# Performance work log

Hardware: AMD Instinct MI355X
Metric: run time of the kernel (lower is better)

## Reference

```python
import jax, jax.numpy as jnp
import numpy as np

B = 16384
D1 = 256
D2 = 256
D_FF = 1024
N_BINS = 16
TAIL = 3.0
MIN_VAL = 1e-3
MIN_TOTAL = N_BINS * MIN_VAL
TAIL_CONST = float(np.log(np.exp(1.0 - MIN_VAL) - 1.0))
D_OUT = (3 * N_BINS - 1) * D2  # 12032


def setup_inputs() -> dict:
    key = jax.random.key(0)
    ks = jax.random.split(key, 8)
    s = lambda fan: 1.0 / np.sqrt(fan)
    return {
        'x1': jax.random.normal(ks[0], (B, D1), jnp.float32),
        'x2': jax.random.normal(ks[1], (B, D2), jnp.float32),
        'W0': jax.random.normal(ks[2], (D1, D_FF), jnp.float32) * s(D1),
        'b0': jnp.zeros((D_FF,), jnp.float32),
        'W1': jax.random.normal(ks[3], (D_FF, D_FF), jnp.float32) * s(D_FF),
        'b1': jnp.zeros((D_FF,), jnp.float32),
        'W2': jax.random.normal(ks[4], (D_FF, D_OUT), jnp.float32) * s(D_FF),
        'b2': jnp.zeros((D_OUT,), jnp.float32),
    }


def _rqs_forward(x, wu, hu, du):
    # x: [B, D2]; wu, hu: [B, D2, N_BINS]; du: [B, D2, N_BINS-1]
    widths = MIN_VAL + (1.0 - MIN_TOTAL) * jax.nn.softmax(wu, axis=-1)
    heights = MIN_VAL + (1.0 - MIN_TOTAL) * jax.nn.softmax(hu, axis=-1)
    cw = jnp.cumsum(widths, axis=-1)
    cw = jnp.concatenate([jnp.zeros_like(cw[..., :1]), cw], axis=-1)
    cw = 2.0 * TAIL * cw - TAIL  # x bin edges in [-TAIL, TAIL], [B,D2,N_BINS+1]
    ch = jnp.cumsum(heights, axis=-1)
    ch = jnp.concatenate([jnp.zeros_like(ch[..., :1]), ch], axis=-1)
    ch = 2.0 * TAIL * ch - TAIL  # y bin edges
    w = cw[..., 1:] - cw[..., :-1]
    h = ch[..., 1:] - ch[..., :-1]
    # boundary derivatives padded so softplus(TAIL_CONST)+MIN_VAL == 1 (linear tails)
    pad = jnp.full_like(du[..., :1], TAIL_CONST)
    d = MIN_VAL + jax.nn.softplus(jnp.concatenate([pad, du, pad], axis=-1))  # [B,D2,N_BINS+1]
    inside = (x > -TAIL) & (x < TAIL)
    xc = jnp.clip(x, -TAIL, TAIL)
    # data-dependent bin search against interior edges
    idx = jnp.sum((xc[..., None] >= cw[..., 1:-1]).astype(jnp.int32), axis=-1)  # [B,D2]
    take = lambda a: jnp.take_along_axis(a, idx[..., None], axis=-1)[..., 0]
    xk = take(cw[..., :-1]); yk = take(ch[..., :-1])
    wk = take(w); hk = take(h)
    dk = take(d[..., :-1]); dk1 = take(d[..., 1:])
    sk = hk / wk
    theta = (xc - xk) / wk
    t1m = theta * (1.0 - theta)
    denom = sk + (dk + dk1 - 2.0 * sk) * t1m
    y = yk + hk * (sk * theta * theta + dk * t1m) / denom
    deriv = sk * sk * (dk1 * theta * theta + 2.0 * sk * t1m + dk * (1.0 - theta) ** 2) / (denom * denom)
    y = jnp.where(inside, y, x)            # identity tails
    logdet = jnp.where(inside, jnp.log(deriv), 0.0)
    return y, jnp.sum(logdet, axis=-1)     # [B,D2], [B]


def reference(x1, x2, W0, b0, W1, b1, W2, b2):
    # conditioner MLP: x1 -> spline parameters
    hdn = jax.nn.relu(x1 @ W0 + b0)
    hdn = jax.nn.relu(hdn @ W1 + b1)
    p = (hdn @ W2 + b2).reshape(-1, D2, 3 * N_BINS - 1)
    wu = p[..., :N_BINS]
    hu = p[..., N_BINS:2 * N_BINS]
    du = p[..., 2 * N_BINS:]
    y2, logdet = _rqs_forward(x2, wu, hu, du)
    return y2, logdet
```

## Files before the change

kernel.cpp:

```cpp
#include <hip/hip_runtime.h>
#include <math.h>

using u16 = unsigned short;
using bf16x8 = __attribute__((ext_vector_type(8))) short;
using f32x4  = __attribute__((ext_vector_type(4))) float;

#define DEV static __device__ __forceinline__

DEV u16 f2bf(float f) {
  union { float f; unsigned u; } v; v.f = f;
  unsigned u = v.u + 0x7fffu + ((v.u >> 16) & 1u);
  return (u16)(u >> 16);
}

DEV void gload16(const void* g, void* l) {
  __builtin_amdgcn_global_load_lds(
      (const __attribute__((address_space(1))) void*)g,
      (__attribute__((address_space(3))) void*)l, 16, 0, 0);
}

__global__ void k_conv_bf16(const float* __restrict__ in, u16* __restrict__ out, int n) {
  int i = blockIdx.x * 256 + threadIdx.x;
  if (i < n) out[i] = f2bf(in[i]);
}

__global__ void k_transconv(const float* __restrict__ in, u16* __restrict__ out,
                            int K, int Nin, int Nout, int pack) {
  __shared__ float t[32][33];
  int kb = blockIdx.x * 32, nb = blockIdx.y * 32;
  int tx = threadIdx.x & 31, ty = threadIdx.x >> 5;
  #pragma unroll
  for (int i = 0; i < 4; ++i) {
    int k = kb + ty + i * 8;
    int no = nb + tx;
    float v = 0.f;
    if (k < K && no < Nout) {
      if (pack) {
        int r = no % 48;
        if (r < 47) v = in[(size_t)k * Nin + (no / 48) * 47 + r];
      } else {
        v = in[(size_t)k * Nin + no];
      }
    }
    t[ty + i * 8][tx] = v;
  }
  __syncthreads();
  #pragma unroll
  for (int i = 0; i < 4; ++i) {
    int no = nb + ty + i * 8;
    int k = kb + tx;
    if (no < Nout && k < K) out[(size_t)no * K + k] = f2bf(t[tx][ty + i * 8]);
  }
}

__global__ __launch_bounds__(256)
void k_gemm_relu(const u16* __restrict__ A, const u16* __restrict__ Bt,
                 const float* __restrict__ bias, u16* __restrict__ C,
                 int N, int K) {
  constexpr int BM = 128, BN = 128, BK = 32;
  __shared__ __align__(16) u16 lds[(BM + BN) * BK];
  int tid = threadIdx.x, w = tid >> 6, lane = tid & 63;
  int bn = blockIdx.x, bm = blockIdx.y;
  int brow = bm * BM, bcol = bn * BN;
  int wm = w >> 1, wn = w & 1;
  int fr = lane & 15, fg = lane >> 4;
  f32x4 acc[4][4];
  #pragma unroll
  for (int i = 0; i < 4; ++i)
    #pragma unroll
    for (int j = 0; j < 4; ++j) acc[i][j] = (f32x4){0.f, 0.f, 0.f, 0.f};

  constexpr int ACH = BM * BK / 8;
  constexpr int CALLS = (BM + BN) * BK / 8 / 64;

  for (int kt = 0; kt < K; kt += BK) {
    for (int j = 0; j * 4 + w < CALLS; ++j) {
      int cb = (j * 4 + w) * 64;
      int c = cb + lane;
      const u16* g;
      if (c < ACH) {
        int row = c >> 2, c8 = c & 3;
        g = A + (size_t)(brow + row) * K + kt + c8 * 8;
      } else {
        int b = c - ACH;
        int nn = b >> 2, c8 = b & 3;
        g = Bt + (size_t)(bcol + nn) * K + kt + c8 * 8;
      }
      gload16(g, &lds[cb * 8]);
    }
    asm volatile("s_waitcnt vmcnt(0)" ::: "memory");
    __syncthreads();

    const u16* Al = lds;
    const u16* Bl = lds + BM * BK;
    bf16x8 af[4], bfr[4];
    #pragma unroll
    for (int mi = 0; mi < 4; ++mi)
      af[mi] = *(const bf16x8*)&Al[(wm * 64 + mi * 16 + fr) * BK + fg * 8];
    #pragma unroll
    for (int ni = 0; ni < 4; ++ni)
      bfr[ni] = *(const bf16x8*)&Bl[(wn * 64 + ni * 16 + fr) * BK + fg * 8];
    #pragma unroll
    for (int mi = 0; mi < 4; ++mi)
      #pragma unroll
      for (int ni = 0; ni < 4; ++ni)
        acc[mi][ni] = __builtin_amdgcn_mfma_f32_16x16x32_bf16(af[mi], bfr[ni], acc[mi][ni], 0, 0, 0);
    __syncthreads();
  }

  #pragma unroll
  for (int ni = 0; ni < 4; ++ni) {
    int col = bcol + wn * 64 + ni * 16 + fr;
    float bb = bias[col];
    #pragma unroll
    for (int mi = 0; mi < 4; ++mi) {
      #pragma unroll
      for (int q = 0; q < 4; ++q) {
        int row = brow + wm * 64 + mi * 16 + fg * 4 + q;
        float vv = acc[mi][ni][q] + bb;
        C[(size_t)row * N + col] = f2bf(vv > 0.f ? vv : 0.f);
      }
    }
  }
}

__global__ __launch_bounds__(256, 2)
void k_gemm3_fused(const u16* __restrict__ A, const u16* __restrict__ Bt,
                   const float* __restrict__ b2, const float* __restrict__ x2,
                   float* __restrict__ y2, float* __restrict__ ldpart) {
  extern __shared__ char smem[];
  const int tid = threadIdx.x, w = tid >> 6, lane = tid & 63;
  const int wm = w >> 1, wn = w & 1;
  const int fr = lane & 15, fg = lane >> 4;

  const int bid = blockIdx.x;
  const int bm = bid >> 6;
  const int bn = ((bid & 7) << 3) | ((bid >> 3) & 7);
  const int brow = bm * 128;

  const int csrc = (tid & 7) ^ ((tid >> 3) & 7);
  const u16* gA[4]; const u16* gB[6];
  #pragma unroll
  for (int k = 0; k < 4; ++k)
    gA[k] = A + (size_t)(brow + (tid >> 3) + 32 * k) * 1024 + csrc * 8;
  #pragma unroll
  for (int k = 0; k < 6; ++k)
    gB[k] = Bt + (size_t)(bn * 192 + (tid >> 3) + 32 * k) * 1024 + csrc * 8;

#define ISSUE_ALL(t1) {                                               \
    const size_t ko_ = (size_t)(t1) * 64;                             \
    char* pa_ = smem + ((t1) & 1) * 16384;                            \
    char* pb_ = smem + 32768 + ((t1) & 1) * 24576;                    \
    gload16(gA[0] + ko_, pa_ + tid * 16);                             \
    gload16(gA[1] + ko_, pa_ + tid * 16 + 4096);                      \
    gload16(gA[2] + ko_, pa_ + tid * 16 + 8192);                      \
    gload16(gA[3] + ko_, pa_ + tid * 16 + 12288);                     \
    gload16(gB[0] + ko_, pb_ + tid * 16);                             \
    gload16(gB[1] + ko_, pb_ + tid * 16 + 4096);                      \
    gload16(gB[2] + ko_, pb_ + tid * 16 + 8192);                      \
    gload16(gB[3] + ko_, pb_ + tid * 16 + 12288);                     \
    gload16(gB[4] + ko_, pb_ + tid * 16 + 16384);                     \
    gload16(gB[5] + ko_, pb_ + tid * 16 + 20480); }

  const int sc0 = ((fg ^ (fr & 7)) << 4);
  const int sc1 = (((4 + fg) ^ (fr & 7)) << 4);

  f32x4 acc[4][6];
  #pragma unroll
  for (int m = 0; m < 4; ++m)
    #pragma unroll
    for (int n = 0; n < 6; ++n) acc[m][n] = (f32x4){0.f, 0.f, 0.f, 0.f};

  ISSUE_ALL(0);
  asm volatile("s_waitcnt vmcnt(0)" ::: "memory");
  __syncthreads();

  for (int t = 0; t < 16; ++t) {
    if (t < 15) ISSUE_ALL(t + 1);
    const char* Ab = smem + (t & 1) * 16384;
    const char* Bb = smem + 32768 + (t & 1) * 24576;
    bf16x8 b0[6], b1[6];
    #pragma unroll
    for (int n = 0; n < 6; ++n) {
      const char* bp = Bb + (wn * 96 + n * 16 + fr) * 128;
      b0[n] = *(const bf16x8*)(bp + sc0);
      b1[n] = *(const bf16x8*)(bp + sc1);
    }
    __builtin_amdgcn_s_setprio(1);
    #pragma unroll
    for (int m = 0; m < 4; ++m) {
      const char* ap = Ab + (wm * 64 + m * 16 + fr) * 128;
      bf16x8 a0 = *(const bf16x8*)(ap + sc0);
      bf16x8 a1 = *(const bf16x8*)(ap + sc1);
      #pragma unroll
      for (int n = 0; n < 6; ++n) {
        acc[m][n] = __builtin_amdgcn_mfma_f32_16x16x32_bf16(a0, b0[n], acc[m][n], 0, 0, 0);
        acc[m][n] = __builtin_amdgcn_mfma_f32_16x16x32_bf16(a1, b1[n], acc[m][n], 0, 0, 0);
      }
    }
    __builtin_amdgcn_s_setprio(0);
    asm volatile("s_waitcnt vmcnt(0)" ::: "memory");
    __syncthreads();
  }

  float* ldacc = (float*)(smem + 50176);
  float* fl = (float*)smem;
  #pragma unroll
  for (int rh = 0; rh < 2; ++rh) {
    if (wm == rh) {
      #pragma unroll
      for (int m = 0; m < 4; ++m)
        #pragma unroll
        for (int n = 0; n < 6; ++n) {
          const int g = wn * 2 + (n >= 3 ? 1 : 0);
          const int ci = (n % 3) * 16 + fr;
          #pragma unroll
          for (int q = 0; q < 4; ++q)
            fl[g * 3136 + (m * 16 + fg * 4 + q) * 49 + ci] = acc[m][n][q];
        }
    }
    __syncthreads();
    {
      const int g = tid >> 6, r = tid & 63;
      const float* pr = fl + g * 3136 + r * 49;
      const int grow = brow + rh * 64 + r;
      const int d2 = bn * 4 + g;
      const float* bb = b2 + (size_t)d2 * 47;

      float wv[16], hv[16];
      #pragma unroll
      for (int j = 0; j < 16; ++j) wv[j] = pr[j] + bb[j];
      #pragma unroll
      for (int j = 0; j < 16; ++j) hv[j] = pr[16 + j] + bb[16 + j];

      float x = x2[(size_t)grow * 256 + d2];
      float xc = fminf(fmaxf(x, -3.f), 3.f);

      float mw = wv[0];
      #pragma unroll
      for (int j = 1; j < 16; ++j) mw = fmaxf(mw, wv[j]);
      float sw = 0.f;
      #pragma unroll
      for (int j = 0; j < 16; ++j) { wv[j] = __expf(wv[j] - mw); sw += wv[j]; }
      float scw = 0.984f / sw;

      float mh = hv[0];
      #pragma unroll
      for (int j = 1; j < 16; ++j) mh = fmaxf(mh, hv[j]);
      float sh = 0.f;
      #pragma unroll
      for (int j = 0; j < 16; ++j) { hv[j] = __expf(hv[j] - mh); sh += hv[j]; }
      float sch = 0.984f / sh;

      int idx = 0;
      float xk = -3.f, cum = 0.f;
      #pragma unroll
      for (int i = 1; i <= 15; ++i) {
        cum += 0.001f + wv[i - 1] * scw;
        float cwi = 6.f * cum - 3.f;
        if (xc >= cwi) { idx = i; xk = cwi; }
      }
      float yk = -3.f, cumh = 0.f;
      #pragma unroll
      for (int i = 1; i <= 15; ++i) {
        cumh += 0.001f + hv[i - 1] * sch;
        float chi = 6.f * cumh - 3.f;
        if (i == idx) yk = chi;
      }
      float wk = 1.f, hk = 1.f;
      #pragma unroll
      for (int i = 0; i < 16; ++i) {
        if (i == idx) {
          wk = 6.f * (0.001f + wv[i] * scw);
          hk = 6.f * (0.001f + hv[i] * sch);
        }
      }
      float dk = 1.f, dk1 = 1.f;
      #pragma unroll
      for (int i = 1; i <= 15; ++i) {
        float u = pr[32 + i - 1] + bb[32 + i - 1];
        float e = __expf(u);
        float dd = 0.001f + (u > 15.f ? u : log1pf(e));
        if (i == idx) dk = dd;
        if (i == idx + 1) dk1 = dd;
      }

      float sk = hk / wk;
      float th = (xc - xk) / wk;
      float om = 1.f - th;
      float t1m = th * om;
      float den = sk + (dk + dk1 - 2.f * sk) * t1m;
      float y = yk + hk * (sk * th * th + dk * t1m) / den;
      float deriv = sk * sk * (dk1 * th * th + 2.f * sk * t1m + dk * om * om) / (den * den);
      bool inside = (x > -3.f) && (x < 3.f);
      float yout = inside ? y : x;
      float ld = inside ? __logf(deriv) : 0.f;

      y2[(size_t)grow * 256 + d2] = yout;
      ldacc[(rh * 64 + r) * 4 + g] = ld;
    }
    __syncthreads();
  }

  if (tid < 128) {
    float s = ldacc[tid * 4] + ldacc[tid * 4 + 1] + ldacc[tid * 4 + 2] + ldacc[tid * 4 + 3];
    ldpart[(size_t)bn * 16384 + brow + tid] = s;
  }
}

__global__ void k_reduce_ld(const float* __restrict__ part, float* __restrict__ out) {
  int r = blockIdx.x * 256 + threadIdx.x;
  float s = 0.f;
  for (int j = 0; j < 64; ++j) s += part[(size_t)j * 16384 + r];
  out[r] = s;
}

extern "C" void kernel_launch(void* const* d_in, const int* in_sizes, int n_in,
                              void* d_out, int out_size, void* d_ws, size_t ws_size,
                              hipStream_t stream) {
  const float* x1 = (const float*)d_in[0];
  const float* x2 = (const float*)d_in[1];
  const float* W0 = (const float*)d_in[2];
  const float* b0 = (const float*)d_in[3];
  const float* W1 = (const float*)d_in[4];
  const float* b1 = (const float*)d_in[5];
  const float* W2 = (const float*)d_in[6];
  const float* b2 = (const float*)d_in[7];
  float* y2 = (float*)d_out;
  float* logdet = y2 + (size_t)16384 * 256;

  char* ws = (char*)d_ws;
  u16* W2t = (u16*)ws;
  u16* W0t = (u16*)(ws + 25165824);
  u16* W1t = (u16*)(ws + 25165824 + 524288);
  u16* x1b = (u16*)(ws + 27787264);
  float* ldp = (float*)(ws + 27787264);
  u16* h1  = (u16*)(ws + 36175872);
  u16* h2  = (u16*)(ws + 69730304);

  hipFuncSetAttribute((const void*)k_gemm3_fused,
                      hipFuncAttributeMaxDynamicSharedMemorySize, 81920);

  k_conv_bf16<<<16384, 256, 0, stream>>>(x1, x1b, 16384 * 256);
  k_transconv<<<dim3(8, 32), 256, 0, stream>>>(W0, W0t, 256, 1024, 1024, 0);
  k_transconv<<<dim3(32, 32), 256, 0, stream>>>(W1, W1t, 1024, 1024, 1024, 0);
  k_transconv<<<dim3(32, 384), 256, 0, stream>>>(W2, W2t, 1024, 12032, 12288, 1);

  k_gemm_relu<<<dim3(8, 128), 256, 0, stream>>>(x1b, W0t, b0, h1, 1024, 256);
  k_gemm_relu<<<dim3(8, 128), 256, 0, stream>>>(h1, W1t, b1, h2, 1024, 1024);
  k_gemm3_fused<<<8192, 256, 81920, stream>>>(h2, W2t, b2, x2, y2, ldp);
  k_reduce_ld<<<64, 256, 0, stream>>>(ldp, logdet);
}
```

Baseline: 736.4 us.

## Enlarge GEMM3 tile to 256 rows, load A fragments directly into registers

The fused final GEMM now uses a 256x192 block tile. Each wave owns 64 rows and all 192 columns, so the grid is halved. A fragments are loaded straight from global memory into registers instead of staging through LDS, and only B is double-buffered in shared memory, which cuts LDS use and traffic. The trade-offs are a larger accumulator footprint (48 f32x4 per lane, which raises register pressure and may lower occupancy), A loads that are not hidden behind asynchronous copies, and an epilogue that runs more serialized spline passes per block.

```diff
diff --git a/kernel.cpp b/kernel.cpp
--- a/kernel.cpp
+++ b/kernel.cpp
@@ -130,31 +130,22 @@
                    float* __restrict__ y2, float* __restrict__ ldpart) {
   extern __shared__ char smem[];
   const int tid = threadIdx.x, w = tid >> 6, lane = tid & 63;
-  const int wm = w >> 1, wn = w & 1;
   const int fr = lane & 15, fg = lane >> 4;
 
   const int bid = blockIdx.x;
   const int bm = bid >> 6;
   const int bn = ((bid & 7) << 3) | ((bid >> 3) & 7);
-  const int brow = bm * 128;
+  const int brow = bm * 256;
 
   const int csrc = (tid & 7) ^ ((tid >> 3) & 7);
-  const u16* gA[4]; const u16* gB[6];
-  #pragma unroll
-  for (int k = 0; k < 4; ++k)
-    gA[k] = A + (size_t)(brow + (tid >> 3) + 32 * k) * 1024 + csrc * 8;
+  const u16* gB[6];
   #pragma unroll
   for (int k = 0; k < 6; ++k)
     gB[k] = Bt + (size_t)(bn * 192 + (tid >> 3) + 32 * k) * 1024 + csrc * 8;
 
-#define ISSUE_ALL(t1) {                                               \
+#define ISSUE_B(t1) {                                                 \
     const size_t ko_ = (size_t)(t1) * 64;                             \
-    char* pa_ = smem + ((t1) & 1) * 16384;                            \
-    char* pb_ = smem + 32768 + ((t1) & 1) * 24576;                    \
-    gload16(gA[0] + ko_, pa_ + tid * 16);                             \
-    gload16(gA[1] + ko_, pa_ + tid * 16 + 4096);                      \
-    gload16(gA[2] + ko_, pa_ + tid * 16 + 8192);                      \
-    gload16(gA[3] + ko_, pa_ + tid * 16 + 12288);                     \
+    char* pb_ = smem + ((t1) & 1) * 24576;                            \
     gload16(gB[0] + ko_, pb_ + tid * 16);                             \
     gload16(gB[1] + ko_, pb_ + tid * 16 + 4096);                      \
     gload16(gB[2] + ko_, pb_ + tid * 16 + 8192);                      \
@@ -162,68 +153,78 @@
     gload16(gB[4] + ko_, pb_ + tid * 16 + 16384);                     \
     gload16(gB[5] + ko_, pb_ + tid * 16 + 20480); }
 
+  const u16* gAm[4];
+  #pragma unroll
+  for (int m = 0; m < 4; ++m)
+    gAm[m] = A + (size_t)(brow + w * 64 + m * 16 + fr) * 1024 + fg * 8;
+
   const int sc0 = ((fg ^ (fr & 7)) << 4);
   const int sc1 = (((4 + fg) ^ (fr & 7)) << 4);
 
-  f32x4 acc[4][6];
+  f32x4 acc[4][12];
   #pragma unroll
   for (int m = 0; m < 4; ++m)
     #pragma unroll
-    for (int n = 0; n < 6; ++n) acc[m][n] = (f32x4){0.f, 0.f, 0.f, 0.f};
-
-  ISSUE_ALL(0);
+    for (int n = 0; n < 12; ++n) acc[m][n] = (f32x4){0.f, 0.f, 0.f, 0.f};
+
+  bf16x8 a[4][2];
+
+  ISSUE_B(0);
+  #pragma unroll
+  for (int m = 0; m < 4; ++m) {
+    a[m][0] = *(const bf16x8*)(gAm[m]);
+    a[m][1] = *(const bf16x8*)(gAm[m] + 32);
+  }
   asm volatile("s_waitcnt vmcnt(0)" ::: "memory");
   __syncthreads();
 
   for (int t = 0; t < 16; ++t) {
-    if (t < 15) ISSUE_ALL(t + 1);
-    const char* Ab = smem + (t & 1) * 16384;
-    const char* Bb = smem + 32768 + (t & 1) * 24576;
-    bf16x8 b0[6], b1[6];
-    #pragma unroll
-    for (int n = 0; n < 6; ++n) {
-      const char* bp = Bb + (wn * 96 + n * 16 + fr) * 128;
-      b0[n] = *(const bf16x8*)(bp + sc0);
-      b1[n] = *(const bf16x8*)(bp + sc1);
-    }
+    if (t < 15) ISSUE_B(t + 1);
+    const char* Bb = smem + (t & 1) * 24576;
     __builtin_amdgcn_s_setprio(1);
     #pragma unroll
-    for (int m = 0; m < 4; ++m) {
-      const char* ap = Ab + (wm * 64 + m * 16 + fr) * 128;
-      bf16x8 a0 = *(const bf16x8*)(ap + sc0);
-      bf16x8 a1 = *(const bf16x8*)(ap + sc1);
-      #pragma unroll
-      for (int n = 0; n < 6; ++n) {
-        acc[m][n] = __builtin_amdgcn_mfma_f32_16x16x32_bf16(a0, b0[n], acc[m][n], 0, 0, 0);
-        acc[m][n] = __builtin_amdgcn_mfma_f32_16x16x32_bf16(a1, b1[n], acc[m][n], 0, 0, 0);
+    for (int kk = 0; kk < 2; ++kk) {
+      const int sc = kk ? sc1 : sc0;
+      #pragma unroll
+      for (int n = 0; n < 12; ++n) {
+        bf16x8 b = *(const bf16x8*)(Bb + (n * 16 + fr) * 128 + sc);
+        #pragma unroll
+        for (int m = 0; m < 4; ++m)
+          acc[m][n] = __builtin_amdgcn_mfma_f32_16x16x32_bf16(a[m][kk], b, acc[m][n], 0, 0, 0);
       }
     }
     __builtin_amdgcn_s_setprio(0);
-    asm volatile("s_waitcnt vmcnt(0)" ::: "memory");
-    __syncthreads();
-  }
-
+    if (t < 15) {
+      const size_t ko = (size_t)(t + 1) * 64;
+      #pragma unroll
+      for (int m = 0; m < 4; ++m) {
+        a[m][0] = *(const bf16x8*)(gAm[m] + ko);
+        a[m][1] = *(const bf16x8*)(gAm[m] + ko + 32);
+      }
+      asm volatile("s_waitcnt vmcnt(0)" ::: "memory");
+      __syncthreads();
+    }
+  }
+  __syncthreads();
+
+  float* slot = (float*)smem;
   float* ldacc = (float*)(smem + 50176);
-  float* fl = (float*)smem;
-  #pragma unroll
-  for (int rh = 0; rh < 2; ++rh) {
-    if (wm == rh) {
-      #pragma unroll
-      for (int m = 0; m < 4; ++m)
+  #pragma unroll
+  for (int g = 0; g < 4; ++g) {
+    #pragma unroll
+    for (int m = 0; m < 4; ++m)
+      #pragma unroll
+      for (int j = 0; j < 3; ++j) {
+        const int n = g * 3 + j;
         #pragma unroll
-        for (int n = 0; n < 6; ++n) {
-          const int g = wn * 2 + (n >= 3 ? 1 : 0);
-          const int ci = (n % 3) * 16 + fr;
-          #pragma unroll
-          for (int q = 0; q < 4; ++q)
-            fl[g * 3136 + (m * 16 + fg * 4 + q) * 49 + ci] = acc[m][n][q];
-        }
-    }
+        for (int q = 0; q < 4; ++q)
+          slot[(w * 64 + m * 16 + fg * 4 + q) * 49 + j * 16 + fr] = acc[m][n][q];
+      }
     __syncthreads();
     {
-      const int g = tid >> 6, r = tid & 63;
-      const float* pr = fl + g * 3136 + r * 49;
-      const int grow = brow + rh * 64 + r;
+      const int r = tid;
+      const float* pr = slot + r * 49;
+      const int grow = brow + r;
       const int d2 = bn * 4 + g;
       const float* bb = b2 + (size_t)d2 * 47;
 
@@ -297,12 +298,12 @@
       float ld = inside ? __logf(deriv) : 0.f;
 
       y2[(size_t)grow * 256 + d2] = yout;
-      ldacc[(rh * 64 + r) * 4 + g] = ld;
+      ldacc[r * 4 + g] = ld;
     }
     __syncthreads();
   }
 
-  if (tid < 128) {
+  {
     float s = ldacc[tid * 4] + ldacc[tid * 4 + 1] + ldacc[tid * 4 + 2] + ldacc[tid * 4 + 3];
     ldpart[(size_t)bn * 16384 + brow + tid] = s;
   }
@@ -339,7 +340,7 @@
   u16* h2  = (u16*)(ws + 69730304);
 
   hipFuncSetAttribute((const void*)k_gemm3_fused,
-                      hipFuncAttributeMaxDynamicSharedMemorySize, 81920);
+                      hipFuncAttributeMaxDynamicSharedMemorySize, 54272);
 
   k_conv_bf16<<<16384, 256, 0, stream>>>(x1, x1b, 16384 * 256);
   k_transconv<<<dim3(8, 32), 256, 0, stream>>>(W0, W0t, 256, 1024, 1024, 0);
@@ -348,6 +349,6 @@
 
   k_gemm_relu<<<dim3(8, 128), 256, 0, stream>>>(x1b, W0t, b0, h1, 1024, 256);
   k_gemm_relu<<<dim3(8, 128), 256, 0, stream>>>(h1, W1t, b1, h2, 1024, 1024);
-  k_gemm3_fused<<<8192, 256, 81920, stream>>>(h2, W2t, b2, x2, y2, ldp);
+  k_gemm3_fused<<<4096, 256, 54272, stream>>>(h2, W2t, b2, x2, y2, ldp);
   k_reduce_ld<<<64, 256, 0, stream>>>(ldp, logdet);
 }
```

Result: slower. 752.4 us (+2.2%).

## Halve K-tile in fused GEMM3 to cut LDS and raise occupancy

Applied to the files above, without the earlier changes.

Shrinks the K step of the big output GEMM from 64 to 32, which halves the double-buffered LDS footprint, adjusts the swizzle and global-load mapping to match, and raises launch bounds to 3 blocks per CU. The aim is more resident waves so the memory-bound main loop and the heavy epilogue can hide latency better. In exchange there are twice as many barriers and iterations, and register pressure is tighter with 96 accumulator floats per thread. The epilogue's LDS use must also fit inside the smaller allocation.

```diff
diff --git a/kernel.cpp b/kernel.cpp
--- a/kernel.cpp
+++ b/kernel.cpp
@@ -124,7 +124,7 @@
   }
 }
 
-__global__ __launch_bounds__(256, 2)
+__global__ __launch_bounds__(256, 3)
 void k_gemm3_fused(const u16* __restrict__ A, const u16* __restrict__ Bt,
                    const float* __restrict__ b2, const float* __restrict__ x2,
                    float* __restrict__ y2, float* __restrict__ ldpart) {
@@ -138,32 +138,20 @@
   const int bn = ((bid & 7) << 3) | ((bid >> 3) & 7);
   const int brow = bm * 128;
 
-  const int csrc = (tid & 7) ^ ((tid >> 3) & 7);
-  const u16* gA[4]; const u16* gB[6];
-  #pragma unroll
-  for (int k = 0; k < 4; ++k)
-    gA[k] = A + (size_t)(brow + (tid >> 3) + 32 * k) * 1024 + csrc * 8;
-  #pragma unroll
-  for (int k = 0; k < 6; ++k)
-    gB[k] = Bt + (size_t)(bn * 192 + (tid >> 3) + 32 * k) * 1024 + csrc * 8;
+  const int csrc = (tid & 3) ^ ((tid >> 3) & 3);
+  const u16* gA0 = A + (size_t)(brow + (tid >> 2)) * 1024 + csrc * 8;
+  const u16* gB0 = Bt + (size_t)(bn * 192 + (tid >> 2)) * 1024 + csrc * 8;
 
 #define ISSUE_ALL(t1) {                                               \
-    const size_t ko_ = (size_t)(t1) * 64;                             \
-    char* pa_ = smem + ((t1) & 1) * 16384;                            \
-    char* pb_ = smem + 32768 + ((t1) & 1) * 24576;                    \
-    gload16(gA[0] + ko_, pa_ + tid * 16);                             \
-    gload16(gA[1] + ko_, pa_ + tid * 16 + 4096);                      \
-    gload16(gA[2] + ko_, pa_ + tid * 16 + 8192);                      \
-    gload16(gA[3] + ko_, pa_ + tid * 16 + 12288);                     \
-    gload16(gB[0] + ko_, pb_ + tid * 16);                             \
-    gload16(gB[1] + ko_, pb_ + tid * 16 + 4096);                      \
-    gload16(gB[2] + ko_, pb_ + tid * 16 + 8192);                      \
-    gload16(gB[3] + ko_, pb_ + tid * 16 + 12288);                     \
-    gload16(gB[4] + ko_, pb_ + tid * 16 + 16384);                     \
-    gload16(gB[5] + ko_, pb_ + tid * 16 + 20480); }
-
-  const int sc0 = ((fg ^ (fr & 7)) << 4);
-  const int sc1 = (((4 + fg) ^ (fr & 7)) << 4);
+    const size_t ko_ = (size_t)(t1) * 32;                             \
+    char* p_ = smem + ((t1) & 1) * 20480 + tid * 16;                  \
+    gload16(gA0 + ko_, p_);                                           \
+    gload16(gA0 + 65536 + ko_, p_ + 4096);                            \
+    gload16(gB0 + ko_, p_ + 8192);                                    \
+    gload16(gB0 + 65536 + ko_, p_ + 12288);                           \
+    gload16(gB0 + 131072 + ko_, p_ + 16384); }
+
+  const int sc = ((fg ^ ((fr >> 1) & 3)) << 4);
 
   f32x4 acc[4][6];
   #pragma unroll
@@ -175,28 +163,21 @@
   asm volatile("s_waitcnt vmcnt(0)" ::: "memory");
   __syncthreads();
 
-  for (int t = 0; t < 16; ++t) {
-    if (t < 15) ISSUE_ALL(t + 1);
-    const char* Ab = smem + (t & 1) * 16384;
-    const char* Bb = smem + 32768 + (t & 1) * 24576;
-    bf16x8 b0[6], b1[6];
-    #pragma unroll
-    for (int n = 0; n < 6; ++n) {
-      const char* bp = Bb + (wn * 96 + n * 16 + fr) * 128;
-      b0[n] = *(const bf16x8*)(bp + sc0);
-      b1[n] = *(const bf16x8*)(bp + sc1);
-    }
+  for (int t = 0; t < 32; ++t) {
+    if (t < 31) ISSUE_ALL(t + 1);
+    const char* Ab = smem + (t & 1) * 20480;
+    const char* Bb = Ab + 8192;
+    bf16x8 b[6];
+    #pragma unroll
+    for (int n = 0; n < 6; ++n)
+      b[n] = *(const bf16x8*)(Bb + (wn * 96 + n * 16 + fr) * 64 + sc);
     __builtin_amdgcn_s_setprio(1);
     #pragma unroll
     for (int m = 0; m < 4; ++m) {
-      const char* ap = Ab + (wm * 64 + m * 16 + fr) * 128;
-      bf16x8 a0 = *(const bf16x8*)(ap + sc0);
-      bf16x8 a1 = *(const bf16x8*)(ap + sc1);
-      #pragma unroll
-      for (int n = 0; n < 6; ++n) {
-        acc[m][n] = __builtin_amdgcn_mfma_f32_16x16x32_bf16(a0, b0[n], acc[m][n], 0, 0, 0);
-        acc[m][n] = __builtin_amdgcn_mfma_f32_16x16x32_bf16(a1, b1[n], acc[m][n], 0, 0, 0);
-      }
+      bf16x8 a = *(const bf16x8*)(Ab + (wm * 64 + m * 16 + fr) * 64 + sc);
+      #pragma unroll
+      for (int n = 0; n < 6; ++n)
+        acc[m][n] = __builtin_amdgcn_mfma_f32_16x16x32_bf16(a, b[n], acc[m][n], 0, 0, 0);
     }
     __builtin_amdgcn_s_setprio(0);
     asm volatile("s_waitcnt vmcnt(0)" ::: "memory");
@@ -339,7 +320,7 @@
   u16* h2  = (u16*)(ws + 69730304);
 
   hipFuncSetAttribute((const void*)k_gemm3_fused,
-                      hipFuncAttributeMaxDynamicSharedMemorySize, 81920);
+                      hipFuncAttributeMaxDynamicSharedMemorySize, 52224);
 
   k_conv_bf16<<<16384, 256, 0, stream>>>(x1, x1b, 16384 * 256);
   k_transconv<<<dim3(8, 32), 256, 0, stream>>>(W0, W0t, 256, 1024, 1024, 0);
@@ -348,6 +329,6 @@
 
   k_gemm_relu<<<dim3(8, 128), 256, 0, stream>>>(x1b, W0t, b0, h1, 1024, 256);
   k_gemm_relu<<<dim3(8, 128), 256, 0, stream>>>(h1, W1t, b1, h2, 1024, 1024);
-  k_gemm3_fused<<<8192, 256, 81920, stream>>>(h2, W2t, b2, x2, y2, ldp);
+  k_gemm3_fused<<<8192, 256, 52224, stream>>>(h2, W2t, b2, x2, y2, ldp);
   k_reduce_ld<<<64, 256, 0, stream>>>(ldp, logdet);
 }
```

Measured after the change: 747.3 us. Within noise of the previous version (+1.5%).
